# Performance work log

Measured on AMD Instinct MI355X. Metric: run time of the kernel, lower is better.

The kernel has to match this reference:

```python
import jax, jax.numpy as jnp
import numpy as np

C = 256
HEADS = 4
RADIUS = 2
LN_EPS = 1e-5


def setup_inputs() -> dict:
    key = jax.random.key(0)
    ks = jax.random.split(key, 8)
    s = 0.02
    return {
        "feat": jax.random.normal(ks[0], (8, C, 64, 64), dtype=jnp.float32),
        "in_w": jax.random.normal(ks[1], (3 * C, C), dtype=jnp.float32) * s,
        "in_b": jnp.zeros((3 * C,), dtype=jnp.float32),
        "out_w": jax.random.normal(ks[2], (C, C), dtype=jnp.float32) * s,
        "out_b": jnp.zeros((C,), dtype=jnp.float32),
        "proj_w": jax.random.normal(ks[3], (C, 4 * C), dtype=jnp.float32) * s,
        "proj_b": jnp.zeros((C,), dtype=jnp.float32),
        "ln_g": jnp.ones((C,), dtype=jnp.float32),
        "ln_b": jnp.zeros((C,), dtype=jnp.float32),
    }


def _spatial_mask(h, w, radius):
    yy, xx = jnp.meshgrid(jnp.arange(h), jnp.arange(w), indexing="ij")
    coords = jnp.stack([yy.ravel(), xx.ravel()], axis=-1).astype(jnp.float32)  # [N,2]
    dist = jnp.abs(coords[:, None, :] - coords[None, :, :]).sum(-1)  # Manhattan [N,N]
    return jnp.where(dist > radius, -jnp.inf, 0.0).astype(jnp.float32)


def _attend(qf, mf, mask, in_w, in_b, out_w, out_b, proj_w, proj_b, ln_g, ln_b):
    b, c, h, w = qf.shape
    n = h * w
    d = c // HEADS
    qt = qf.reshape(b, c, n).transpose(0, 2, 1)  # [B,N,C]
    mt = mf.reshape(b, c, n).transpose(0, 2, 1)
    q = qt @ in_w[:c].T + in_b[:c]
    k = mt @ in_w[c:2 * c].T + in_b[c:2 * c]
    v = mt @ in_w[2 * c:].T + in_b[2 * c:]
    # [B,H,N,D]
    q = q.reshape(b, n, HEADS, d).transpose(0, 2, 1, 3)
    k = k.reshape(b, n, HEADS, d).transpose(0, 2, 1, 3)
    v = v.reshape(b, n, HEADS, d).transpose(0, 2, 1, 3)
    scores = jnp.einsum("bhnd,bhmd->bhnm", q, k) / jnp.sqrt(jnp.float32(d)) + mask
    attn = jax.nn.softmax(scores, axis=-1)
    ctx = jnp.einsum("bhnm,bhmd->bhnd", attn, v)
    ctx = ctx.transpose(0, 2, 1, 3).reshape(b, n, c) @ out_w.T + out_b  # [B,N,C]
    asym = jnp.concatenate([qt, ctx, jnp.abs(qt - ctx), qt * ctx], axis=-1)
    y = asym @ proj_w.T + proj_b
    mu = y.mean(-1, keepdims=True)
    var = ((y - mu) ** 2).mean(-1, keepdims=True)
    y = (y - mu) / jnp.sqrt(var + LN_EPS) * ln_g + ln_b
    y = jax.nn.relu(y)
    return y.transpose(0, 2, 1).reshape(b, c, h, w)


def reference(feat, in_w, in_b, out_w, out_b, proj_w, proj_b, ln_g, ln_b):
    b, c, h, w = feat.shape
    mid = w // 2
    left = feat[:, :, :, :mid]
    right = feat[:, :, :, mid:]
    right_mirror = right[:, :, :, ::-1]
    left_mirror = left[:, :, :, ::-1]
    mask = _spatial_mask(h, mid, RADIUS)
    args = (mask, in_w, in_b, out_w, out_b, proj_w, proj_b, ln_g, ln_b)
    left_asym = _attend(left, right_mirror, *args)
    right_asym = _attend(right, left_mirror, *args)
    return jnp.concatenate([left_asym, right_asym], axis=-1)
```

## Files before the change

### kernel.cpp

```cpp
#include <hip/hip_runtime.h>
#include <hip/hip_bf16.h>


#define NTOK 32768

using bf16x8 = __attribute__((ext_vector_type(8))) short;
using f32x4  = __attribute__((ext_vector_type(4))) float;

__device__ __forceinline__ float b2f(short s) {
    unsigned u = ((unsigned)(unsigned short)s) << 16;
    union { unsigned u; float f; } c; c.u = u; return c.f;
}
__device__ __forceinline__ short f2b(float f) {
    __hip_bfloat16 h = __float2bfloat16(f);
    return *(short*)&h;
}
__device__ __forceinline__ void async_copy16(const void* g, void* l) {
    __builtin_amdgcn_global_load_lds(
        (const __attribute__((address_space(1))) unsigned int*)g,
        (__attribute__((address_space(3))) unsigned int*)l, 16, 0, 0);
}

__global__ __launch_bounds__(256) void transpose_cast(const float* __restrict__ feat,
                                                      __hip_bfloat16* __restrict__ X) {
    __shared__ float tile[32][33];
    const int b  = blockIdx.z;
    const int c0 = blockIdx.y * 32;
    const int sp0 = blockIdx.x * 32;
    const int tid = threadIdx.x;
    const int col = tid & 31, rowg = tid >> 5;
    #pragma unroll
    for (int u = 0; u < 4; ++u) {
        int cl = rowg + u * 8;
        tile[cl][col] = feat[((size_t)(b * 256 + c0 + cl) << 12) + sp0 + col];
    }
    __syncthreads();
    #pragma unroll
    for (int u = 0; u < 4; ++u) {
        int spl = rowg + u * 8;
        X[(size_t)(b * 4096 + sp0 + spl) * 256 + c0 + col] = __float2bfloat16(tile[col][spl]);
    }
}

__global__ __launch_bounds__(256) void cast_weights(const float* __restrict__ in_w,
                                                    const float* __restrict__ out_w,
                                                    const float* __restrict__ proj_w,
                                                    __hip_bfloat16* __restrict__ wbf) {
    const int i = blockIdx.x * 256 + threadIdx.x;
    if (i < 196608) wbf[i] = __float2bfloat16(in_w[i]);
    if (i < 65536)  wbf[196608 + i] = __float2bfloat16(out_w[i]);
    if (i < 262144) wbf[262144 + i] = __float2bfloat16(proj_w[i]);
}

template <int KDIM, bool OUT_BF16>
__global__ __launch_bounds__(256) void mfma_gemm(const __hip_bfloat16* __restrict__ A,
                                                 const __hip_bfloat16* __restrict__ W,
                                                 const float* __restrict__ bias,
                                                 void* __restrict__ C, int Ntot) {
    __shared__ __align__(16) short As[128 * 64];
    __shared__ __align__(16) short Bs[128 * 64];
    const int tid = threadIdx.x;
    const int m0 = blockIdx.x * 128;
    const int n0 = blockIdx.y * 128;
    const int wave = tid >> 6, lane = tid & 63;
    const int wm = (wave >> 1) * 64;
    const int wn = (wave & 1) * 64;
    const int fm = lane & 15;
    const int fq = lane >> 4;

    f32x4 acc[4][4] = {};

    for (int k0 = 0; k0 < KDIM; k0 += 64) {
        #pragma unroll
        for (int v = 0; v < 4; ++v) {
            const int qb = v * 256 + wave * 64;
            const int q = qb + lane;
            const int r = q >> 3;
            const int cs = (q & 7) ^ (r & 7);
            async_copy16(A + (size_t)(m0 + r) * KDIM + k0 + cs * 8, &As[qb * 8]);
            async_copy16(W + (size_t)(n0 + r) * KDIM + k0 + cs * 8, &Bs[qb * 8]);
        }
        __syncthreads();
        #pragma unroll
        for (int kk = 0; kk < 2; ++kk) {
            bf16x8 af[4], bw[4];
            #pragma unroll
            for (int i = 0; i < 4; ++i) {
                const int row = wm + i * 16 + fm;
                af[i] = *(const bf16x8*)(&As[row * 64 + (((fq + kk * 4) ^ (fm & 7)) * 8)]);
            }
            #pragma unroll
            for (int j = 0; j < 4; ++j) {
                const int row = wn + j * 16 + fm;
                bw[j] = *(const bf16x8*)(&Bs[row * 64 + (((fq + kk * 4) ^ (fm & 7)) * 8)]);
            }
            #pragma unroll
            for (int i = 0; i < 4; ++i)
                #pragma unroll
                for (int j = 0; j < 4; ++j)
                    acc[i][j] = __builtin_amdgcn_mfma_f32_16x16x32_bf16(af[i], bw[j], acc[i][j], 0, 0, 0);
        }
        __syncthreads();
    }
    #pragma unroll
    for (int j = 0; j < 4; ++j) {
        const int col = n0 + wn + j * 16 + fm;
        const float bv = bias[col];
        #pragma unroll
        for (int i = 0; i < 4; ++i) {
            #pragma unroll
            for (int r = 0; r < 4; ++r) {
                const int row = m0 + wm + i * 16 + fq * 4 + r;
                const float v = acc[i][j][r] + bv;
                if (OUT_BF16)
                    ((__hip_bfloat16*)C)[(size_t)row * Ntot + col] = __float2bfloat16(v);
                else
                    ((float*)C)[(size_t)row * Ntot + col] = v;
            }
        }
    }
}

#define P0DY ((2u)|(2u<<3)|(2u<<6)|(2u<<9)|(2u<<12)|(1u<<15)|(1u<<18)|(1u<<21))
#define P0DX ((2u)|(1u<<3)|(3u<<6)|(0u<<9)|(4u<<12)|(2u<<15)|(1u<<18)|(3u<<21))
#define P1DY ((3u)|(3u<<3)|(3u<<6)|(0u<<9)|(4u<<12)|(2u<<15)|(2u<<18)|(2u<<21))
#define P1DX ((2u)|(1u<<3)|(3u<<6)|(2u<<9)|(2u<<12)|(2u<<15)|(2u<<18)|(2u<<21))

__global__ __launch_bounds__(256) void attn_kernel(const __hip_bfloat16* __restrict__ qkv,
                                                   __hip_bfloat16* __restrict__ ctx) {
    const int t = blockIdx.x * 4 + (threadIdx.x >> 6);
    const int lane = threadIdx.x & 63;
    const int n  = lane >> 3;
    const int cg = lane & 7;
    const int x6 = t & 63;
    const int yq = (t >> 6) & 63;
    const int b  = t >> 12;
    const int side = x6 >> 5;
    const int x = x6 & 31;

    bool valid[2];
    size_t kb[2];
    #pragma unroll
    for (int p = 0; p < 2; ++p) {
        const unsigned dyp = p ? P1DY : P0DY;
        const unsigned dxp = p ? P1DX : P0DX;
        const int sh = 3 * n;
        const int dy = (int)((dyp >> sh) & 7) - 2;
        const int dx = (int)((dxp >> sh) & 7) - 2;
        const int yy = yq + dy, xx = x + dx;
        valid[p] = (p == 0 || n < 5) && yy >= 0 && yy < 64 && xx >= 0 && xx < 32;
        const int xm = side ? (31 - xx) : (63 - xx);
        int tm = (b << 12) + (yy << 6) + xm;
        if (!valid[p]) tm = t;
        kb[p] = (size_t)tm * 768 + 256 + cg * 8;
    }
    const size_t qb = (size_t)t * 768 + cg * 8;
    const size_t ob = (size_t)t * 256;

    #pragma unroll
    for (int hp = 0; hp < 2; ++hp) {
        bf16x8 q8[2], k8[2][2], v8[2][2];
        #pragma unroll
        for (int hh = 0; hh < 2; ++hh) {
            const int h = hp * 2 + hh;
            q8[hh] = *(const bf16x8*)(qkv + qb + h * 64);
            #pragma unroll
            for (int p = 0; p < 2; ++p) {
                k8[hh][p] = *(const bf16x8*)(qkv + kb[p] + h * 64);
                v8[hh][p] = *(const bf16x8*)(qkv + kb[p] + h * 64 + 256);
            }
        }
        #pragma unroll
        for (int hh = 0; hh < 2; ++hh) {
            float sc[2];
            #pragma unroll
            for (int p = 0; p < 2; ++p) {
                float s = 0.f;
                #pragma unroll
                for (int j = 0; j < 8; ++j) s += b2f(q8[hh][j]) * b2f(k8[hh][p][j]);
                s += __shfl_xor(s, 1, 64);
                s += __shfl_xor(s, 2, 64);
                s += __shfl_xor(s, 4, 64);
                sc[p] = valid[p] ? s * 0.125f : -1e30f;
            }
            const float p0 = __expf(sc[0]);
            const float p1 = __expf(sc[1]);
            float l = p0 + p1;
            l += __shfl_xor(l, 8, 64);
            l += __shfl_xor(l, 16, 64);
            l += __shfl_xor(l, 32, 64);

            float o[8];
            #pragma unroll
            for (int j = 0; j < 8; ++j)
                o[j] = p0 * b2f(v8[hh][0][j]) + p1 * b2f(v8[hh][1][j]);
            float r4[4];
            #pragma unroll
            for (int i = 0; i < 4; ++i) {
                const float a = o[2 * i], bb = o[2 * i + 1];
                const float mine = (n & 1) ? bb : a;
                const float theirs = (n & 1) ? a : bb;
                r4[i] = mine + __shfl_xor(theirs, 8, 64);
            }
            float r2[2];
            #pragma unroll
            for (int i = 0; i < 2; ++i) {
                const float a = r2[0] * 0.f + r4[2 * i], bb = r4[2 * i + 1];
                const float mine = (n & 2) ? bb : a;
                const float theirs = (n & 2) ? a : bb;
                r2[i] = mine + __shfl_xor(theirs, 16, 64);
            }
            float ov;
            {
                const float a = r2[0], bb = r2[1];
                const float mine = (n & 4) ? bb : a;
                const float theirs = (n & 4) ? a : bb;
                ov = mine + __shfl_xor(theirs, 32, 64);
            }
            ctx[ob + (hp * 2 + hh) * 64 + cg * 8 + n] = __float2bfloat16(ov / l);
        }
    }
}

__global__ __launch_bounds__(256) void proj_ln_fused(const __hip_bfloat16* __restrict__ X,
                                                     const __hip_bfloat16* __restrict__ C2,
                                                     const __hip_bfloat16* __restrict__ W,
                                                     const float* __restrict__ bias,
                                                     const float* __restrict__ ln_g,
                                                     const float* __restrict__ ln_b,
                                                     float* __restrict__ out) {
    __shared__ __align__(16) short smem[20480];
    __shared__ float mu_s[64], inv_s[64];
    short* As = smem;
    short* Bs = smem + 4096;
    const int tid = threadIdx.x;
    const int m0 = blockIdx.x * 64;
    const int b = m0 >> 12, sp0 = m0 & 4095;
    const int wave = tid >> 6, lane = tid & 63;
    const int wn = wave * 64;
    const int fm = lane & 15;
    const int fq = lane >> 4;

    f32x4 acc[4][4] = {};

    for (int k0 = 0; k0 < 1024; k0 += 64) {
        const int g = k0 >> 8;
        const int cb = k0 & 255;
        #pragma unroll
        for (int v = 0; v < 8; ++v) {
            const int qbu = v * 256 + wave * 64;
            const int q = qbu + lane;
            const int r = q >> 3;
            const int cs = (q & 7) ^ (r & 7);
            async_copy16(W + (size_t)r * 1024 + k0 + cs * 8, &Bs[qbu * 8]);
        }
        if (g == 0) {
            #pragma unroll
            for (int v = 0; v < 2; ++v) {
                const int qbu = v * 256 + wave * 64;
                const int q = qbu + lane;
                const int r = q >> 3;
                const int cs = (q & 7) ^ (r & 7);
                async_copy16(X + (size_t)(m0 + r) * 256 + cb + cs * 8, &As[qbu * 8]);
            }
        } else if (g == 1) {
            #pragma unroll
            for (int v = 0; v < 2; ++v) {
                const int qbu = v * 256 + wave * 64;
                const int q = qbu + lane;
                const int r = q >> 3;
                const int cs = (q & 7) ^ (r & 7);
                async_copy16(C2 + (size_t)(m0 + r) * 256 + cb + cs * 8, &As[qbu * 8]);
            }
        } else {
            #pragma unroll
            for (int v = 0; v < 2; ++v) {
                const int q = v * 256 + tid;
                const int r = q >> 3;
                const int cs = (q & 7) ^ (r & 7);
                const size_t abase = (size_t)(m0 + r) * 256 + cb + cs * 8;
                int4 qraw = *(const int4*)(X + abase);
                int4 craw = *(const int4*)(C2 + abase);
                const short* qs = (const short*)&qraw;
                const short* cw = (const short*)&craw;
                short tmp[8];
                #pragma unroll
                for (int j = 0; j < 8; ++j) {
                    const float qv = b2f(qs[j]), cv = b2f(cw[j]);
                    tmp[j] = f2b(g == 2 ? fabsf(qv - cv) : qv * cv);
                }
                *(int4*)(&As[q * 8]) = *(int4*)tmp;
            }
        }
        __syncthreads();
        #pragma unroll
        for (int kk = 0; kk < 2; ++kk) {
            bf16x8 af[4], bw[4];
            #pragma unroll
            for (int i = 0; i < 4; ++i) {
                const int row = i * 16 + fm;
                af[i] = *(const bf16x8*)(&As[row * 64 + (((fq + kk * 4) ^ (fm & 7)) * 8)]);
            }
            #pragma unroll
            for (int j = 0; j < 4; ++j) {
                const int row = wn + j * 16 + fm;
                bw[j] = *(const bf16x8*)(&Bs[row * 64 + (((fq + kk * 4) ^ (fm & 7)) * 8)]);
            }
            #pragma unroll
            for (int i = 0; i < 4; ++i)
                #pragma unroll
                for (int j = 0; j < 4; ++j)
                    acc[i][j] = __builtin_amdgcn_mfma_f32_16x16x32_bf16(af[i], bw[j], acc[i][j], 0, 0, 0);
        }
        __syncthreads();
    }
    short* ys = smem;
    #pragma unroll
    for (int j = 0; j < 4; ++j) {
        const int col = wn + j * 16 + fm;
        const float bv = bias[col];
        #pragma unroll
        for (int i = 0; i < 4; ++i)
            #pragma unroll
            for (int r = 0; r < 4; ++r)
                ys[(i * 16 + fq * 4 + r) * 266 + col] = f2b(acc[i][j][r] + bv);
    }
    __syncthreads();
    {
        const int tt = tid >> 2, seg = tid & 3;
        float s = 0.f, ss = 0.f;
        #pragma unroll
        for (int j = 0; j < 64; ++j) {
            const float v = b2f(ys[tt * 266 + seg * 64 + j]);
            s += v; ss += v * v;
        }
        s += __shfl_xor(s, 1, 64);  ss += __shfl_xor(ss, 1, 64);
        s += __shfl_xor(s, 2, 64);  ss += __shfl_xor(ss, 2, 64);
        if (seg == 0) {
            const float mu = s * (1.f / 256.f);
            const float var = ss * (1.f / 256.f) - mu * mu;
            mu_s[tt] = mu;
            inv_s[tt] = rsqrtf(var + 1e-5f);
        }
    }
    __syncthreads();
    {
        const int tl = tid & 63;
        const int j0 = tid >> 6;
        const float mu = mu_s[tl], inv = inv_s[tl];
        #pragma unroll
        for (int u = 0; u < 64; ++u) {
            const int j = j0 * 64 + u;
            const float v = (b2f(ys[tl * 266 + j]) - mu) * inv * ln_g[j] + ln_b[j];
            out[((size_t)(b * 256 + j) << 12) + sp0 + tl] = fmaxf(v, 0.f);
        }
    }
}

extern "C" void kernel_launch(void* const* d_in, const int* in_sizes, int n_in,
                              void* d_out, int out_size, void* d_ws, size_t ws_size,
                              hipStream_t stream) {
    (void)in_sizes; (void)n_in; (void)out_size; (void)ws_size;
    const float* feat   = (const float*)d_in[0];
    const float* in_w   = (const float*)d_in[1];
    const float* in_b   = (const float*)d_in[2];
    const float* out_w  = (const float*)d_in[3];
    const float* out_b  = (const float*)d_in[4];
    const float* proj_w = (const float*)d_in[5];
    const float* proj_b = (const float*)d_in[6];
    const float* ln_g   = (const float*)d_in[7];
    const float* ln_b   = (const float*)d_in[8];
    float* out = (float*)d_out;

    char* ws = (char*)d_ws;
    __hip_bfloat16* Xbf  = (__hip_bfloat16*)(ws);
    __hip_bfloat16* wbf  = (__hip_bfloat16*)(ws + (size_t)(16) * (1 << 20));
    __hip_bfloat16* qkv  = (__hip_bfloat16*)(ws + (size_t)(17) * (1 << 20));
    __hip_bfloat16* ctx  = (__hip_bfloat16*)(ws + (size_t)(65) * (1 << 20));
    __hip_bfloat16* ctx2 = (__hip_bfloat16*)(ws + (size_t)(81) * (1 << 20));
    __hip_bfloat16* in_wbf   = wbf;
    __hip_bfloat16* out_wbf  = wbf + 196608;
    __hip_bfloat16* proj_wbf = wbf + 262144;

    transpose_cast<<<dim3(128, 8, 8), 256, 0, stream>>>(feat, Xbf);
    cast_weights  <<<1024, 256, 0, stream>>>(in_w, out_w, proj_w, wbf);
    mfma_gemm<256, true><<<dim3(256, 6), 256, 0, stream>>>(Xbf, in_wbf, in_b, qkv, 768);
    attn_kernel   <<<NTOK / 4, 256, 0, stream>>>(qkv, ctx);
    mfma_gemm<256, true><<<dim3(256, 2), 256, 0, stream>>>(ctx, out_wbf, out_b, ctx2, 256);
    proj_ln_fused <<<NTOK / 64, 256, 0, stream>>>(Xbf, ctx2, proj_wbf, proj_b,
                                                  ln_g, ln_b, out);
}
```

Before: 197.5 us.

## Merge prep kernels and widen GEMM tiles to 512-thread blocks

```diff
diff --git a/kernel.cpp b/kernel.cpp
--- a/kernel.cpp
+++ b/kernel.cpp
@@ -21,50 +21,52 @@
         (__attribute__((address_space(3))) unsigned int*)l, 16, 0, 0);
 }
 
-__global__ __launch_bounds__(256) void transpose_cast(const float* __restrict__ feat,
-                                                      __hip_bfloat16* __restrict__ X) {
-    __shared__ float tile[32][33];
-    const int b  = blockIdx.z;
-    const int c0 = blockIdx.y * 32;
-    const int sp0 = blockIdx.x * 32;
+__global__ __launch_bounds__(256) void prep_kernel(const float* __restrict__ feat,
+                                                   const float* __restrict__ in_w,
+                                                   const float* __restrict__ out_w,
+                                                   const float* __restrict__ proj_w,
+                                                   __hip_bfloat16* __restrict__ X,
+                                                   __hip_bfloat16* __restrict__ wbf) {
+    const int bid = blockIdx.x;
     const int tid = threadIdx.x;
-    const int col = tid & 31, rowg = tid >> 5;
-    #pragma unroll
-    for (int u = 0; u < 4; ++u) {
-        int cl = rowg + u * 8;
-        tile[cl][col] = feat[((size_t)(b * 256 + c0 + cl) << 12) + sp0 + col];
-    }
-    __syncthreads();
-    #pragma unroll
-    for (int u = 0; u < 4; ++u) {
-        int spl = rowg + u * 8;
-        X[(size_t)(b * 4096 + sp0 + spl) * 256 + c0 + col] = __float2bfloat16(tile[col][spl]);
-    }
-}
-
-__global__ __launch_bounds__(256) void cast_weights(const float* __restrict__ in_w,
-                                                    const float* __restrict__ out_w,
-                                                    const float* __restrict__ proj_w,
-                                                    __hip_bfloat16* __restrict__ wbf) {
-    const int i = blockIdx.x * 256 + threadIdx.x;
-    if (i < 196608) wbf[i] = __float2bfloat16(in_w[i]);
-    if (i < 65536)  wbf[196608 + i] = __float2bfloat16(out_w[i]);
-    if (i < 262144) wbf[262144 + i] = __float2bfloat16(proj_w[i]);
+    if (bid < 8192) {
+        __shared__ float tile[32][33];
+        const int sp0 = (bid & 127) * 32;
+        const int c0  = ((bid >> 7) & 7) * 32;
+        const int b   = bid >> 10;
+        const int col = tid & 31, rowg = tid >> 5;
+        #pragma unroll
+        for (int u = 0; u < 4; ++u) {
+            int cl = rowg + u * 8;
+            tile[cl][col] = feat[((size_t)(b * 256 + c0 + cl) << 12) + sp0 + col];
+        }
+        __syncthreads();
+        #pragma unroll
+        for (int u = 0; u < 4; ++u) {
+            int spl = rowg + u * 8;
+            X[(size_t)(b * 4096 + sp0 + spl) * 256 + c0 + col] = __float2bfloat16(tile[col][spl]);
+        }
+    } else {
+        const int i = (bid - 8192) * 256 + tid;
+        if (i < 196608) wbf[i] = __float2bfloat16(in_w[i]);
+        if (i < 65536)  wbf[196608 + i] = __float2bfloat16(out_w[i]);
+        if (i < 262144) wbf[262144 + i] = __float2bfloat16(proj_w[i]);
+    }
 }
 
 template <int KDIM, bool OUT_BF16>
-__global__ __launch_bounds__(256) void mfma_gemm(const __hip_bfloat16* __restrict__ A,
+__global__ __launch_bounds__(512) void mfma_gemm(const __hip_bfloat16* __restrict__ A,
                                                  const __hip_bfloat16* __restrict__ W,
                                                  const float* __restrict__ bias,
                                                  void* __restrict__ C, int Ntot) {
     __shared__ __align__(16) short As[128 * 64];
-    __shared__ __align__(16) short Bs[128 * 64];
+    __shared__ __align__(16) short Bs[256 * 64];
     const int tid = threadIdx.x;
     const int m0 = blockIdx.x * 128;
-    const int n0 = blockIdx.y * 128;
+    const int n0 = blockIdx.y * 256;
     const int wave = tid >> 6, lane = tid & 63;
-    const int wm = (wave >> 1) * 64;
-    const int wn = (wave & 1) * 64;
+    const int wm = (wave >> 2) * 64;
+    const int wn = (wave & 3) * 64;
     const int fm = lane & 15;
     const int fq = lane >> 4;
 
@@ -72,12 +74,19 @@
 
     for (int k0 = 0; k0 < KDIM; k0 += 64) {
         #pragma unroll
-        for (int v = 0; v < 4; ++v) {
-            const int qb = v * 256 + wave * 64;
+        for (int v = 0; v < 2; ++v) {
+            const int qb = v * 512 + wave * 64;
             const int q = qb + lane;
             const int r = q >> 3;
             const int cs = (q & 7) ^ (r & 7);
             async_copy16(A + (size_t)(m0 + r) * KDIM + k0 + cs * 8, &As[qb * 8]);
+        }
+        #pragma unroll
+        for (int v = 0; v < 4; ++v) {
+            const int qb = v * 512 + wave * 64;
+            const int q = qb + lane;
+            const int r = q >> 3;
+            const int cs = (q & 7) ^ (r & 7);
             async_copy16(W + (size_t)(n0 + r) * KDIM + k0 + cs * 8, &Bs[qb * 8]);
         }
         __syncthreads();
@@ -205,7 +214,7 @@
             float r2[2];
             #pragma unroll
             for (int i = 0; i < 2; ++i) {
-                const float a = r2[0] * 0.f + r4[2 * i], bb = r4[2 * i + 1];
+                const float a = r4[2 * i], bb = r4[2 * i + 1];
                 const float mine = (n & 2) ? bb : a;
                 const float theirs = (n & 2) ? a : bb;
                 r2[i] = mine + __shfl_xor(theirs, 16, 64);
@@ -222,22 +231,23 @@
     }
 }
 
-__global__ __launch_bounds__(256) void proj_ln_fused(const __hip_bfloat16* __restrict__ X,
+__global__ __launch_bounds__(512) void proj_ln_fused(const __hip_bfloat16* __restrict__ X,
                                                      const __hip_bfloat16* __restrict__ C2,
                                                      const __hip_bfloat16* __restrict__ W,
                                                      const float* __restrict__ bias,
                                                      const float* __restrict__ ln_g,
                                                      const float* __restrict__ ln_b,
                                                      float* __restrict__ out) {
-    __shared__ __align__(16) short smem[20480];
-    __shared__ float mu_s[64], inv_s[64];
+    __shared__ __align__(16) short smem[34048];
+    __shared__ float mu_s[128], inv_s[128];
     short* As = smem;
-    short* Bs = smem + 4096;
+    short* Bs = smem + 8192;
     const int tid = threadIdx.x;
-    const int m0 = blockIdx.x * 64;
+    const int m0 = blockIdx.x * 128;
     const int b = m0 >> 12, sp0 = m0 & 4095;
     const int wave = tid >> 6, lane = tid & 63;
-    const int wn = wave * 64;
+    const int wm = (wave >> 2) * 64;
+    const int wn = (wave & 3) * 64;
     const int fm = lane & 15;
     const int fq = lane >> 4;
 
@@ -247,35 +257,35 @@
         const int g = k0 >> 8;
         const int cb = k0 & 255;
         #pragma unroll
-        for (int v = 0; v < 8; ++v) {
-            const int qbu = v * 256 + wave * 64;
-            const int q = qbu + lane;
+        for (int v = 0; v < 4; ++v) {
+            const int qb = v * 512 + wave * 64;
+            const int q = qb + lane;
             const int r = q >> 3;
             const int cs = (q & 7) ^ (r & 7);
-            async_copy16(W + (size_t)r * 1024 + k0 + cs * 8, &Bs[qbu * 8]);
+            async_copy16(W + (size_t)r * 1024 + k0 + cs * 8, &Bs[qb * 8]);
         }
         if (g == 0) {
             #pragma unroll
             for (int v = 0; v < 2; ++v) {
-                const int qbu = v * 256 + wave * 64;
-                const int q = qbu + lane;
+                const int qb = v * 512 + wave * 64;
+                const int q = qb + lane;
                 const int r = q >> 3;
                 const int cs = (q & 7) ^ (r & 7);
-                async_copy16(X + (size_t)(m0 + r) * 256 + cb + cs * 8, &As[qbu * 8]);
+                async_copy16(X + (size_t)(m0 + r) * 256 + cb + cs * 8, &As[qb * 8]);
             }
         } else if (g == 1) {
             #pragma unroll
             for (int v = 0; v < 2; ++v) {
-                const int qbu = v * 256 + wave * 64;
-                const int q = qbu + lane;
+                const int qb = v * 512 + wave * 64;
+                const int q = qb + lane;
                 const int r = q >> 3;
                 const int cs = (q & 7) ^ (r & 7);
-                async_copy16(C2 + (size_t)(m0 + r) * 256 + cb + cs * 8, &As[qbu * 8]);
+                async_copy16(C2 + (size_t)(m0 + r) * 256 + cb + cs * 8, &As[qb * 8]);
             }
         } else {
             #pragma unroll
             for (int v = 0; v < 2; ++v) {
-                const int q = v * 256 + tid;
+                const int q = v * 512 + tid;
                 const int r = q >> 3;
                 const int cs = (q & 7) ^ (r & 7);
                 const size_t abase = (size_t)(m0 + r) * 256 + cb + cs * 8;
@@ -298,7 +308,7 @@
             bf16x8 af[4], bw[4];
             #pragma unroll
             for (int i = 0; i < 4; ++i) {
-                const int row = i * 16 + fm;
+                const int row = wm + i * 16 + fm;
                 af[i] = *(const bf16x8*)(&As[row * 64 + (((fq + kk * 4) ^ (fm & 7)) * 8)]);
             }
             #pragma unroll
@@ -323,7 +333,7 @@
         for (int i = 0; i < 4; ++i)
             #pragma unroll
             for (int r = 0; r < 4; ++r)
-                ys[(i * 16 + fq * 4 + r) * 266 + col] = f2b(acc[i][j][r] + bv);
+                ys[(wm + i * 16 + fq * 4 + r) * 266 + col] = f2b(acc[i][j][r] + bv);
     }
     __syncthreads();
     {
@@ -345,8 +355,8 @@
     }
     __syncthreads();
     {
-        const int tl = tid & 63;
-        const int j0 = tid >> 6;
+        const int tl = tid & 127;
+        const int j0 = tid >> 7;
         const float mu = mu_s[tl], inv = inv_s[tl];
         #pragma unroll
         for (int u = 0; u < 64; ++u) {
@@ -382,11 +392,10 @@
     __hip_bfloat16* out_wbf  = wbf + 196608;
     __hip_bfloat16* proj_wbf = wbf + 262144;
 
-    transpose_cast<<<dim3(128, 8, 8), 256, 0, stream>>>(feat, Xbf);
-    cast_weights  <<<1024, 256, 0, stream>>>(in_w, out_w, proj_w, wbf);
-    mfma_gemm<256, true><<<dim3(256, 6), 256, 0, stream>>>(Xbf, in_wbf, in_b, qkv, 768);
+    prep_kernel   <<<9216, 256, 0, stream>>>(feat, in_w, out_w, proj_w, Xbf, wbf);
+    mfma_gemm<256, true><<<dim3(256, 3), 512, 0, stream>>>(Xbf, in_wbf, in_b, qkv, 768);
     attn_kernel   <<<NTOK / 4, 256, 0, stream>>>(qkv, ctx);
-    mfma_gemm<256, true><<<dim3(256, 2), 256, 0, stream>>>(ctx, out_wbf, out_b, ctx2, 256);
-    proj_ln_fused <<<NTOK / 64, 256, 0, stream>>>(Xbf, ctx2, proj_wbf, proj_b,
-                                                  ln_g, ln_b, out);
-}
+    mfma_gemm<256, true><<<dim3(256, 1), 512, 0, stream>>>(ctx, out_wbf, out_b, ctx2, 256);
+    proj_ln_fused <<<NTOK / 128, 512, 0, stream>>>(Xbf, ctx2, proj_wbf, proj_b,
+                                                   ln_g, ln_b, out);
+}
```

Result: no change. 200.6 us (+1.6%).

## Fuse out-projection GEMM into proj+LayerNorm kernel and merge prep kernels

Applied to the files above, without the earlier changes.

```diff
diff --git a/kernel.cpp b/kernel.cpp
--- a/kernel.cpp
+++ b/kernel.cpp
@@ -21,35 +21,37 @@
         (__attribute__((address_space(3))) unsigned int*)l, 16, 0, 0);
 }
 
-__global__ __launch_bounds__(256) void transpose_cast(const float* __restrict__ feat,
-                                                      __hip_bfloat16* __restrict__ X) {
-    __shared__ float tile[32][33];
-    const int b  = blockIdx.z;
-    const int c0 = blockIdx.y * 32;
-    const int sp0 = blockIdx.x * 32;
+__global__ __launch_bounds__(256) void prep_kernel(const float* __restrict__ feat,
+                                                   const float* __restrict__ in_w,
+                                                   const float* __restrict__ out_w,
+                                                   const float* __restrict__ proj_w,
+                                                   __hip_bfloat16* __restrict__ X,
+                                                   __hip_bfloat16* __restrict__ wbf) {
+    const int bid = blockIdx.x;
     const int tid = threadIdx.x;
-    const int col = tid & 31, rowg = tid >> 5;
-    #pragma unroll
-    for (int u = 0; u < 4; ++u) {
-        int cl = rowg + u * 8;
-        tile[cl][col] = feat[((size_t)(b * 256 + c0 + cl) << 12) + sp0 + col];
-    }
-    __syncthreads();
-    #pragma unroll
-    for (int u = 0; u < 4; ++u) {
-        int spl = rowg + u * 8;
-        X[(size_t)(b * 4096 + sp0 + spl) * 256 + c0 + col] = __float2bfloat16(tile[col][spl]);
-    }
-}
-
-__global__ __launch_bounds__(256) void cast_weights(const float* __restrict__ in_w,
-                                                    const float* __restrict__ out_w,
-                                                    const float* __restrict__ proj_w,
-                                                    __hip_bfloat16* __restrict__ wbf) {
-    const int i = blockIdx.x * 256 + threadIdx.x;
-    if (i < 196608) wbf[i] = __float2bfloat16(in_w[i]);
-    if (i < 65536)  wbf[196608 + i] = __float2bfloat16(out_w[i]);
-    if (i < 262144) wbf[262144 + i] = __float2bfloat16(proj_w[i]);
+    if (bid < 8192) {
+        __shared__ float tile[32][33];
+        const int sp0 = (bid & 127) * 32;
+        const int c0  = ((bid >> 7) & 7) * 32;
+        const int b   = bid >> 10;
+        const int col = tid & 31, rowg = tid >> 5;
+        #pragma unroll
+        for (int u = 0; u < 4; ++u) {
+            int cl = rowg + u * 8;
+            tile[cl][col] = feat[((size_t)(b * 256 + c0 + cl) << 12) + sp0 + col];
+        }
+        __syncthreads();
+        #pragma unroll
+        for (int u = 0; u < 4; ++u) {
+            int spl = rowg + u * 8;
+            X[(size_t)(b * 4096 + sp0 + spl) * 256 + c0 + col] = __float2bfloat16(tile[col][spl]);
+        }
+    } else {
+        const int i = (bid - 8192) * 256 + tid;
+        if (i < 196608) wbf[i] = __float2bfloat16(in_w[i]);
+        if (i < 65536)  wbf[196608 + i] = __float2bfloat16(out_w[i]);
+        if (i < 262144) wbf[262144 + i] = __float2bfloat16(proj_w[i]);
+    }
 }
 
 template <int KDIM, bool OUT_BF16>
@@ -205,7 +207,7 @@
             float r2[2];
             #pragma unroll
             for (int i = 0; i < 2; ++i) {
-                const float a = r2[0] * 0.f + r4[2 * i], bb = r4[2 * i + 1];
+                const float a = r4[2 * i], bb = r4[2 * i + 1];
                 const float mine = (n & 2) ? bb : a;
                 const float theirs = (n & 2) ? a : bb;
                 r2[i] = mine + __shfl_xor(theirs, 16, 64);
@@ -217,22 +219,26 @@
                 const float theirs = (n & 4) ? a : bb;
                 ov = mine + __shfl_xor(theirs, 32, 64);
             }
-            ctx[ob + (hp * 2 + hh) * 64 + cg * 8 + n] = __float2bfloat16(ov / l);
+            const float rl = __builtin_amdgcn_rcpf(l);
+            ctx[ob + (hp * 2 + hh) * 64 + cg * 8 + n] = __float2bfloat16(ov * rl);
         }
     }
 }
 
 __global__ __launch_bounds__(256) void proj_ln_fused(const __hip_bfloat16* __restrict__ X,
-                                                     const __hip_bfloat16* __restrict__ C2,
+                                                     const __hip_bfloat16* __restrict__ CTX,
+                                                     const __hip_bfloat16* __restrict__ W2,
+                                                     const float* __restrict__ out_b,
                                                      const __hip_bfloat16* __restrict__ W,
                                                      const float* __restrict__ bias,
                                                      const float* __restrict__ ln_g,
                                                      const float* __restrict__ ln_b,
                                                      float* __restrict__ out) {
-    __shared__ __align__(16) short smem[20480];
+    __shared__ __align__(16) short smem[36864];
     __shared__ float mu_s[64], inv_s[64];
-    short* As = smem;
-    short* Bs = smem + 4096;
+    short* c2s = smem;
+    short* As  = smem + 16384;
+    short* Bs  = smem + 20480;
     const int tid = threadIdx.x;
     const int m0 = blockIdx.x * 64;
     const int b = m0 >> 12, sp0 = m0 & 4095;
@@ -241,8 +247,65 @@
     const int fm = lane & 15;
     const int fq = lane >> 4;
 
+    {
+        f32x4 acc2[4][4] = {};
+        for (int k0 = 0; k0 < 256; k0 += 64) {
+            #pragma unroll
+            for (int v = 0; v < 2; ++v) {
+                const int qbu = v * 256 + wave * 64;
+                const int q = qbu + lane;
+                const int r = q >> 3;
+                const int cs = (q & 7) ^ (r & 7);
+                async_copy16(CTX + (size_t)(m0 + r) * 256 + k0 + cs * 8, &As[qbu * 8]);
+            }
+            #pragma unroll
+            for (int v = 0; v < 8; ++v) {
+                const int qbu = v * 256 + wave * 64;
+                const int q = qbu + lane;
+                const int r = q >> 3;
+                const int cs = (q & 7) ^ (r & 7);
+                async_copy16(W2 + (size_t)r * 256 + k0 + cs * 8, &Bs[qbu * 8]);
+            }
+            __syncthreads();
+            #pragma unroll
+            for (int kk = 0; kk < 2; ++kk) {
+                bf16x8 af[4], bw[4];
+                #pragma unroll
+                for (int i = 0; i < 4; ++i) {
+                    const int row = i * 16 + fm;
+                    af[i] = *(const bf16x8*)(&As[row * 64 + (((fq + kk * 4) ^ (fm & 7)) * 8)]);
+                }
+                #pragma unroll
+                for (int j = 0; j < 4; ++j) {
+                    const int row = wn + j * 16 + fm;
+                    bw[j] = *(const bf16x8*)(&Bs[row * 64 + (((fq + kk * 4) ^ (fm & 7)) * 8)]);
+                }
+                #pragma unroll
+                for (int i = 0; i < 4; ++i)
+                    #pragma unroll
+                    for (int j = 0; j < 4; ++j)
+                        acc2[i][j] = __builtin_amdgcn_mfma_f32_16x16x32_bf16(af[i], bw[j], acc2[i][j], 0, 0, 0);
+            }
+            __syncthreads();
+        }
+        #pragma unroll
+        for (int j = 0; j < 4; ++j) {
+            const int col = wn + j * 16 + fm;
+            const float bv = out_b[col];
+            const int jch = col >> 3, cl = col & 7;
+            #pragma unroll
+            for (int i = 0; i < 4; ++i)
+                #pragma unroll
+                for (int rr = 0; rr < 4; ++rr) {
+                    const int row = i * 16 + fq * 4 + rr;
+                    const int slot = (jch & 24) | ((jch & 7) ^ (row & 7));
+                    c2s[row * 256 + slot * 8 + cl] = f2b(acc2[i][j][rr] + bv);
+                }
+        }
+    }
+    __syncthreads();
+
     f32x4 acc[4][4] = {};
-
     for (int k0 = 0; k0 < 1024; k0 += 64) {
         const int g = k0 >> 8;
         const int cb = k0 & 255;
@@ -263,24 +326,16 @@
                 const int cs = (q & 7) ^ (r & 7);
                 async_copy16(X + (size_t)(m0 + r) * 256 + cb + cs * 8, &As[qbu * 8]);
             }
-        } else if (g == 1) {
-            #pragma unroll
-            for (int v = 0; v < 2; ++v) {
-                const int qbu = v * 256 + wave * 64;
-                const int q = qbu + lane;
-                const int r = q >> 3;
-                const int cs = (q & 7) ^ (r & 7);
-                async_copy16(C2 + (size_t)(m0 + r) * 256 + cb + cs * 8, &As[qbu * 8]);
-            }
-        } else {
+        } else if (g >= 2) {
             #pragma unroll
             for (int v = 0; v < 2; ++v) {
                 const int q = v * 256 + tid;
                 const int r = q >> 3;
                 const int cs = (q & 7) ^ (r & 7);
-                const size_t abase = (size_t)(m0 + r) * 256 + cb + cs * 8;
-                int4 qraw = *(const int4*)(X + abase);
-                int4 craw = *(const int4*)(C2 + abase);
+                int4 qraw = *(const int4*)(X + (size_t)(m0 + r) * 256 + cb + cs * 8);
+                const int jch = (cb >> 3) + cs;
+                const int slot = (jch & 24) | ((jch & 7) ^ (r & 7));
+                int4 craw = *(const int4*)(&c2s[r * 256 + slot * 8]);
                 const short* qs = (const short*)&qraw;
                 const short* cw = (const short*)&craw;
                 short tmp[8];
@@ -296,10 +351,20 @@
         #pragma unroll
         for (int kk = 0; kk < 2; ++kk) {
             bf16x8 af[4], bw[4];
-            #pragma unroll
-            for (int i = 0; i < 4; ++i) {
-                const int row = i * 16 + fm;
-                af[i] = *(const bf16x8*)(&As[row * 64 + (((fq + kk * 4) ^ (fm & 7)) * 8)]);
+            if (g == 1) {
+                #pragma unroll
+                for (int i = 0; i < 4; ++i) {
+                    const int row = i * 16 + fm;
+                    const int jch = (cb >> 3) + fq + kk * 4;
+                    const int slot = (jch & 24) | ((jch & 7) ^ (row & 7));
+                    af[i] = *(const bf16x8*)(&c2s[row * 256 + slot * 8]);
+                }
+            } else {
+                #pragma unroll
+                for (int i = 0; i < 4; ++i) {
+                    const int row = i * 16 + fm;
+                    af[i] = *(const bf16x8*)(&As[row * 64 + (((fq + kk * 4) ^ (fm & 7)) * 8)]);
+                }
             }
             #pragma unroll
             for (int j = 0; j < 4; ++j) {
@@ -314,7 +379,7 @@
         }
         __syncthreads();
     }
-    short* ys = smem;
+    short* ys = smem + 16384;
     #pragma unroll
     for (int j = 0; j < 4; ++j) {
         const int col = wn + j * 16 + fm;
@@ -377,16 +442,13 @@
     __hip_bfloat16* wbf  = (__hip_bfloat16*)(ws + (size_t)(16) * (1 << 20));
     __hip_bfloat16* qkv  = (__hip_bfloat16*)(ws + (size_t)(17) * (1 << 20));
     __hip_bfloat16* ctx  = (__hip_bfloat16*)(ws + (size_t)(65) * (1 << 20));
-    __hip_bfloat16* ctx2 = (__hip_bfloat16*)(ws + (size_t)(81) * (1 << 20));
     __hip_bfloat16* in_wbf   = wbf;
     __hip_bfloat16* out_wbf  = wbf + 196608;
     __hip_bfloat16* proj_wbf = wbf + 262144;
 
-    transpose_cast<<<dim3(128, 8, 8), 256, 0, stream>>>(feat, Xbf);
-    cast_weights  <<<1024, 256, 0, stream>>>(in_w, out_w, proj_w, wbf);
+    prep_kernel   <<<9216, 256, 0, stream>>>(feat, in_w, out_w, proj_w, Xbf, wbf);
     mfma_gemm<256, true><<<dim3(256, 6), 256, 0, stream>>>(Xbf, in_wbf, in_b, qkv, 768);
     attn_kernel   <<<NTOK / 4, 256, 0, stream>>>(qkv, ctx);
-    mfma_gemm<256, true><<<dim3(256, 2), 256, 0, stream>>>(ctx, out_wbf, out_b, ctx2, 256);
-    proj_ln_fused <<<NTOK / 64, 256, 0, stream>>>(Xbf, ctx2, proj_wbf, proj_b,
-                                                  ln_g, ln_b, out);
-}
+    proj_ln_fused <<<NTOK / 64, 256, 0, stream>>>(Xbf, ctx, out_wbf, out_b,
+                                                  proj_wbf, proj_b, ln_g, ln_b, out);
+}
```

Result: faster. 185.7 us (-6.0%).
